# Kernel tuning notes

Measured on AMD Instinct MI355X. Metric: run time of the kernel, lower is better.

## Reference

```python
import jax, jax.numpy as jnp
import numpy as np

SEQ = 4096
EMB = 2048
DQ = 2048
DV = 2048

def setup_inputs() -> dict:
    key = jax.random.key(0)
    k1, k2, k3, k4 = jax.random.split(key, 4)
    scale = 1.0 / np.sqrt(EMB)
    return {
        "embedding_word": jax.random.normal(k1, (SEQ, EMB), dtype=jnp.float32),
        "w_q": jax.random.normal(k2, (DQ, EMB), dtype=jnp.float32) * scale,
        "w_k": jax.random.normal(k3, (DQ, EMB), dtype=jnp.float32) * scale,
        "w_v": jax.random.normal(k4, (DV, EMB), dtype=jnp.float32) * scale,
    }

def reference(embedding_word, w_q, w_k, w_v):
    # nn.Linear: y = x @ W.T (bias=False)
    q = embedding_word @ w_q.T            # [S, d_q]
    k = embedding_word @ w_k.T            # [S, d_q]
    v = embedding_word @ w_v.T            # [S, d_v]
    scores = q @ k.T                      # [S, S]
    S = scores.shape[0]
    causal = jnp.tril(jnp.ones((S, S), dtype=bool))  # True = keep
    masked = jnp.where(causal, scores, -jnp.inf)
    weights = jax.nn.softmax(masked / jnp.sqrt(jnp.float32(DQ)), axis=-1)
    return weights @ v                    # [S, d_v]
```

## Files before the change

kernel.cpp:

```cpp
#include <hip/hip_runtime.h>


using u16 = unsigned short;
typedef __bf16 bf16x8 __attribute__((ext_vector_type(8)));
typedef float  f32x4  __attribute__((ext_vector_type(4)));
typedef u16    u16x8  __attribute__((ext_vector_type(8)));

__device__ __forceinline__ u16 f2b(float f) {
  union { float f; unsigned u; } x; x.f = f;
  unsigned r = x.u + 0x7fffu + ((x.u >> 16) & 1u);
  return (u16)(r >> 16);
}
__device__ __forceinline__ float b2f(u16 h) {
  union { unsigned u; float f; } x; x.u = ((unsigned)h) << 16;
  return x.f;
}

#define GLL16(src, dst)                                                        \
  __builtin_amdgcn_global_load_lds(                                            \
      (const __attribute__((address_space(1))) void*)(src),                    \
      (__attribute__((address_space(3))) void*)(dst), 16, 0, 0)

#define MFMA_BF16(a, b, c) __builtin_amdgcn_mfma_f32_16x16x32_bf16(a, b, c, 0, 0, 0)

__global__ __launch_bounds__(256)
void cast_all(const float* __restrict__ x, const float* __restrict__ wq,
              const float* __restrict__ wk, const float* __restrict__ wv,
              u16* __restrict__ dst) {
  const int b = blockIdx.x;
  const float* src;
  size_t off;
  if (b < 4096)      { src = x;  off = (size_t)b * 2048; }
  else if (b < 6144) { src = wq; off = (size_t)(b - 4096) * 2048; }
  else if (b < 8192) { src = wk; off = (size_t)(b - 6144) * 2048; }
  else               { src = wv; off = (size_t)(b - 8192) * 2048; }
  const size_t e = off + (size_t)threadIdx.x * 8;
  float4 a = *(const float4*)(src + e);
  float4 c = *(const float4*)(src + e + 4);
  u16x8 o;
  o[0] = f2b(a.x); o[1] = f2b(a.y); o[2] = f2b(a.z); o[3] = f2b(a.w);
  o[4] = f2b(c.x); o[5] = f2b(c.y); o[6] = f2b(c.z); o[7] = f2b(c.w);
  *(u16x8*)(dst + (size_t)b * 2048 + (size_t)threadIdx.x * 8) = o;
}

__global__ __launch_bounds__(512)
void gemm_qk256(const u16* __restrict__ A, const u16* __restrict__ W,
                u16* __restrict__ Qo, u16* __restrict__ Ko) {
  extern __shared__ char lds[];
  constexpr int NT = 32;
  const int bn = blockIdx.x, bm = blockIdx.y;
  const int tid = threadIdx.x;
  const int w = tid >> 6, lane = tid & 63;
  const int wr = w >> 2, wc = w & 3;
  const int l15 = lane & 15, l4 = lane >> 4;
  const int rs = lane >> 3;
  const int csw = ((lane & 7) ^ rs) << 3;
  const int m0 = bm * 256, n0 = bn * 256;

  const u16* gA = A + (size_t)(m0 + w * 8 + rs) * 2048 + csw;
  const u16* gB = W + (size_t)(n0 + w * 8 + rs) * 2048 + csw;
  char* lw = lds + w * 1024;
  const u16* sm = (const u16*)lds;

  auto stA = [&](int p, int u, int tt) {
    GLL16(gA + (size_t)(u * 64) * 2048 + tt * 64, lw + p * 65536 + u * 8192);
  };
  auto stB = [&](int p, int u, int tt) {
    GLL16(gB + (size_t)(u * 64) * 2048 + tt * 64,
          lw + p * 65536 + 32768 + u * 8192);
  };
  const int swz = (l15 & 7) << 3;
  auto rdA = [&](int p, int m, int kk) -> bf16x8 {
    int u = wr * 2 + (m >> 2);
    int r64 = (m & 3) * 16 + l15;
    int e = p * 32768 + u * 4096 + ((r64 * 64 + kk * 32 + l4 * 8) ^ swz);
    return *(const bf16x8*)&sm[e];
  };
  auto rdB = [&](int p, int n, int kk) -> bf16x8 {
    int e = p * 32768 + 16384 + wc * 4096 +
            (((n * 16 + l15) * 64 + kk * 32 + l4 * 8) ^ swz);
    return *(const bf16x8*)&sm[e];
  };

  f32x4 acc[8][4] = {};
  bf16x8 a0[4][2], a1[4][2], b0[2][2], b1[2][2];

  stA(0,0,0); stA(0,1,0); stA(0,2,0); stA(0,3,0);
  stB(0,0,0); stB(0,1,0); stB(0,2,0); stB(0,3,0);
  stA(1,0,1); stA(1,1,1); stA(1,2,1); stA(1,3,1);
  stB(1,0,1); stB(1,1,1); stB(1,2,1); stB(1,3,1);
  asm volatile("s_waitcnt vmcnt(8)" ::: "memory");
  __builtin_amdgcn_sched_barrier(0);
  __builtin_amdgcn_s_barrier();

  for (int t = 0; t < NT; ++t) {
    const int p = t & 1;
    const bool pre = (t + 2 < NT);
#pragma unroll
    for (int m = 0; m < 4; ++m) { a0[m][0] = rdA(p, m, 0); a0[m][1] = rdA(p, m, 1); }
#pragma unroll
    for (int n = 0; n < 2; ++n) { b0[n][0] = rdB(p, n, 0); b0[n][1] = rdB(p, n, 1); }
    __builtin_amdgcn_s_barrier();
    asm volatile("s_waitcnt lgkmcnt(0)" ::: "memory");
    __builtin_amdgcn_sched_barrier(0);
    __builtin_amdgcn_s_setprio(1);
#pragma unroll
    for (int m = 0; m < 4; ++m)
#pragma unroll
      for (int n = 0; n < 2; ++n)
#pragma unroll
        for (int kk = 0; kk < 2; ++kk)
          acc[m][n] = MFMA_BF16(a0[m][kk], b0[n][kk], acc[m][n]);
    __builtin_amdgcn_s_setprio(0);
    __builtin_amdgcn_s_barrier();
    if (pre) { stA(p, 0, t + 2); stA(p, 2, t + 2); }
#pragma unroll
    for (int n = 0; n < 2; ++n) { b1[n][0] = rdB(p, n + 2, 0); b1[n][1] = rdB(p, n + 2, 1); }
    __builtin_amdgcn_s_barrier();
    asm volatile("s_waitcnt lgkmcnt(0)" ::: "memory");
    __builtin_amdgcn_sched_barrier(0);
    __builtin_amdgcn_s_setprio(1);
#pragma unroll
    for (int m = 0; m < 4; ++m)
#pragma unroll
      for (int n = 0; n < 2; ++n)
#pragma unroll
        for (int kk = 0; kk < 2; ++kk)
          acc[m][n + 2] = MFMA_BF16(a0[m][kk], b1[n][kk], acc[m][n + 2]);
    __builtin_amdgcn_s_setprio(0);
    __builtin_amdgcn_s_barrier();
    if (pre) { stB(p, 0, t + 2); stB(p, 1, t + 2); }
#pragma unroll
    for (int m = 0; m < 4; ++m) { a1[m][0] = rdA(p, m + 4, 0); a1[m][1] = rdA(p, m + 4, 1); }
    __builtin_amdgcn_s_barrier();
    asm volatile("s_waitcnt lgkmcnt(0)" ::: "memory");
    __builtin_amdgcn_sched_barrier(0);
    __builtin_amdgcn_s_setprio(1);
#pragma unroll
    for (int m = 0; m < 4; ++m)
#pragma unroll
      for (int n = 0; n < 2; ++n)
#pragma unroll
        for (int kk = 0; kk < 2; ++kk)
          acc[m + 4][n] = MFMA_BF16(a1[m][kk], b0[n][kk], acc[m + 4][n]);
    __builtin_amdgcn_s_setprio(0);
    __builtin_amdgcn_s_barrier();
    if (pre) { stA(p, 1, t + 2); stA(p, 3, t + 2); stB(p, 2, t + 2); stB(p, 3, t + 2); }
    __builtin_amdgcn_s_setprio(1);
#pragma unroll
    for (int m = 0; m < 4; ++m)
#pragma unroll
      for (int n = 0; n < 2; ++n)
#pragma unroll
        for (int kk = 0; kk < 2; ++kk)
          acc[m + 4][n + 2] = MFMA_BF16(a1[m][kk], b1[n][kk], acc[m + 4][n + 2]);
    __builtin_amdgcn_s_setprio(0);
    if (pre)                { asm volatile("s_waitcnt vmcnt(8)" ::: "memory"); }
    else if (t + 1 < NT)    { asm volatile("s_waitcnt vmcnt(0)" ::: "memory"); }
    __builtin_amdgcn_sched_barrier(0);
    __builtin_amdgcn_s_barrier();
  }

  const int row0 = m0 + wr * 128 + l4 * 4;
  if (bn < 8) {
    const int cg0 = bn * 256 + wc * 64 + l15;
#pragma unroll
    for (int m = 0; m < 8; ++m)
#pragma unroll
      for (int n = 0; n < 4; ++n)
#pragma unroll
        for (int j = 0; j < 4; ++j)
          Qo[(size_t)(row0 + m * 16 + j) * 2048 + cg0 + n * 16] = f2b(acc[m][n][j]);
  } else {
    const int cg0 = bn * 256 - 2048 + wc * 64 + l15;
#pragma unroll
    for (int m = 0; m < 8; ++m)
#pragma unroll
      for (int n = 0; n < 4; ++n)
#pragma unroll
        for (int j = 0; j < 4; ++j)
          Ko[(size_t)(row0 + m * 16 + j) * 2048 + cg0 + n * 16] = f2b(acc[m][n][j]);
  }
}

__global__ __launch_bounds__(512)
void gemm_qkv(const u16* __restrict__ A, const u16* __restrict__ W,
              u16* __restrict__ Qo, u16* __restrict__ Ko,
              u16* __restrict__ VTo, int bn_base) {
  extern __shared__ char lds[];
  constexpr int NT = 32;
  const int bn = blockIdx.x + bn_base, bm = blockIdx.y;
  const int tid = threadIdx.x;
  const int w = tid >> 6, lane = tid & 63;
  const int wr = w >> 1, wc = w & 1;
  const int l15 = lane & 15, l4 = lane >> 4;
  const int rs = lane >> 3;
  const int csw = ((lane & 7) ^ rs) << 3;
  const int m0 = bm * 256, n0 = bn * 128;

  const u16* gA = A + (size_t)(m0 + w * 8 + rs) * 2048 + csw;
  const u16* gB = W + (size_t)(n0 + w * 8 + rs) * 2048 + csw;
  char* lw = lds + w * 1024;
  const u16* sm = (const u16*)lds;

  auto stA = [&](int p, int u, int tt) {
    GLL16(gA + (size_t)u * 64 * 2048 + tt * 64, lw + p * 49152 + u * 8192);
  };
  auto stB = [&](int p, int u, int tt) {
    GLL16(gB + (size_t)u * 64 * 2048 + tt * 64, lw + p * 49152 + 32768 + u * 8192);
  };
  const int swz = (l15 & 7) << 3;
  auto rdA = [&](int p, int m, int kk) -> bf16x8 {
    int e = p * 24576 + wr * 4096 + (((m * 16 + l15) * 64 + kk * 32 + l4 * 8) ^ swz);
    return *(const bf16x8*)&sm[e];
  };
  auto rdB = [&](int p, int n, int kk) -> bf16x8 {
    int e = p * 24576 + 16384 + wc * 4096 +
            (((n * 16 + l15) * 64 + kk * 32 + l4 * 8) ^ swz);
    return *(const bf16x8*)&sm[e];
  };

  f32x4 acc[4][4] = {};
  bf16x8 aE[4][2], aO[4][2], b01E[2][2], b01O[2][2], b23E[2][2], b23O[2][2];

  stA(0,0,0); stA(0,1,0); stA(0,2,0); stA(0,3,0); stB(0,0,0); stB(0,1,0);
  stA(1,0,1); stA(1,1,1); stA(1,2,1); stA(1,3,1); stB(1,0,1); stB(1,1,1);
  asm volatile("s_waitcnt vmcnt(6)" ::: "memory");
  __builtin_amdgcn_sched_barrier(0);
  __builtin_amdgcn_s_barrier();
#pragma unroll
  for (int m = 0; m < 4; ++m) { aE[m][0] = rdA(0,m,0); aE[m][1] = rdA(0,m,1); }
#pragma unroll
  for (int n = 0; n < 2; ++n) { b01E[n][0] = rdB(0,n,0); b01E[n][1] = rdB(0,n,1); }
  asm volatile("s_waitcnt lgkmcnt(0)" ::: "memory");
  __builtin_amdgcn_sched_barrier(0);
  __builtin_amdgcn_s_barrier();

  for (int i = 0; i < NT / 2; ++i) {
    const int te = 2 * i, to = 2 * i + 1;
    if (te + 2 < NT) { stA(0,0,te+2); stA(0,1,te+2); stA(0,2,te+2); }
#pragma unroll
    for (int n = 0; n < 2; ++n) { b23E[n][0] = rdB(0,n+2,0); b23E[n][1] = rdB(0,n+2,1); }
    __builtin_amdgcn_s_barrier();
    __builtin_amdgcn_s_setprio(1);
#pragma unroll
    for (int m = 0; m < 4; ++m)
#pragma unroll
      for (int n = 0; n < 2; ++n)
#pragma unroll
        for (int kk = 0; kk < 2; ++kk)
          acc[m][n] = MFMA_BF16(aE[m][kk], b01E[n][kk], acc[m][n]);
    __builtin_amdgcn_s_setprio(0);
    asm volatile("s_waitcnt lgkmcnt(0)" ::: "memory");
    __builtin_amdgcn_sched_barrier(0);
    __builtin_amdgcn_s_barrier();
    if (te + 2 < NT) {
      stA(0,3,te+2); stB(0,0,te+2); stB(0,1,te+2);
      asm volatile("s_waitcnt vmcnt(6)" ::: "memory");
    } else {
      asm volatile("s_waitcnt vmcnt(0)" ::: "memory");
    }
    __builtin_amdgcn_sched_barrier(0);
    __builtin_amdgcn_s_barrier();
#pragma unroll
    for (int m = 0; m < 4; ++m) { aO[m][0] = rdA(1,m,0); aO[m][1] = rdA(1,m,1); }
#pragma unroll
    for (int n = 0; n < 2; ++n) { b01O[n][0] = rdB(1,n,0); b01O[n][1] = rdB(1,n,1); }
    __builtin_amdgcn_s_setprio(1);
#pragma unroll
    for (int m = 0; m < 4; ++m)
#pragma unroll
      for (int n = 0; n < 2; ++n)
#pragma unroll
        for (int kk = 0; kk < 2; ++kk)
          acc[m][n+2] = MFMA_BF16(aE[m][kk], b23E[n][kk], acc[m][n+2]);
    __builtin_amdgcn_s_setprio(0);
    asm volatile("s_waitcnt lgkmcnt(0)" ::: "memory");
    __builtin_amdgcn_sched_barrier(0);
    __builtin_amdgcn_s_barrier();
    if (to + 2 < NT) { stA(1,0,to+2); stA(1,1,to+2); stA(1,2,to+2); }
#pragma unroll
    for (int n = 0; n < 2; ++n) { b23O[n][0] = rdB(1,n+2,0); b23O[n][1] = rdB(1,n+2,1); }
    __builtin_amdgcn_s_barrier();
    __builtin_amdgcn_s_setprio(1);
#pragma unroll
    for (int m = 0; m < 4; ++m)
#pragma unroll
      for (int n = 0; n < 2; ++n)
#pragma unroll
        for (int kk = 0; kk < 2; ++kk)
          acc[m][n] = MFMA_BF16(aO[m][kk], b01O[n][kk], acc[m][n]);
    __builtin_amdgcn_s_setprio(0);
    asm volatile("s_waitcnt lgkmcnt(0)" ::: "memory");
    __builtin_amdgcn_sched_barrier(0);
    __builtin_amdgcn_s_barrier();
    if (to + 2 < NT) {
      stA(1,3,to+2); stB(1,0,to+2); stB(1,1,to+2);
      asm volatile("s_waitcnt vmcnt(6)" ::: "memory");
    } else if (to + 1 < NT) {
      asm volatile("s_waitcnt vmcnt(0)" ::: "memory");
    }
    __builtin_amdgcn_sched_barrier(0);
    __builtin_amdgcn_s_barrier();
    if (to + 1 < NT) {
#pragma unroll
      for (int m = 0; m < 4; ++m) { aE[m][0] = rdA(0,m,0); aE[m][1] = rdA(0,m,1); }
#pragma unroll
      for (int n = 0; n < 2; ++n) { b01E[n][0] = rdB(0,n,0); b01E[n][1] = rdB(0,n,1); }
    }
    __builtin_amdgcn_s_setprio(1);
#pragma unroll
    for (int m = 0; m < 4; ++m)
#pragma unroll
      for (int n = 0; n < 2; ++n)
#pragma unroll
        for (int kk = 0; kk < 2; ++kk)
          acc[m][n+2] = MFMA_BF16(aO[m][kk], b23O[n][kk], acc[m][n+2]);
    __builtin_amdgcn_s_setprio(0);
    asm volatile("s_waitcnt lgkmcnt(0)" ::: "memory");
    __builtin_amdgcn_sched_barrier(0);
    __builtin_amdgcn_s_barrier();
  }

  const int row0 = m0 + wr * 64 + l4 * 4;
  const int cg0 = n0 + wc * 64 + l15;
  if (bn < 16) {
#pragma unroll
    for (int m = 0; m < 4; ++m)
#pragma unroll
      for (int n = 0; n < 4; ++n)
#pragma unroll
        for (int j = 0; j < 4; ++j)
          Qo[(size_t)(row0 + m * 16 + j) * 2048 + cg0 + n * 16] = f2b(acc[m][n][j]);
  } else if (bn < 32) {
#pragma unroll
    for (int m = 0; m < 4; ++m)
#pragma unroll
      for (int n = 0; n < 4; ++n)
#pragma unroll
        for (int j = 0; j < 4; ++j)
          Ko[(size_t)(row0 + m * 16 + j) * 2048 + (cg0 + n * 16 - 2048)] = f2b(acc[m][n][j]);
  } else {
#pragma unroll
    for (int m = 0; m < 4; ++m)
#pragma unroll
      for (int n = 0; n < 4; ++n)
#pragma unroll
        for (int j = 0; j < 4; ++j)
          VTo[(size_t)(cg0 + n * 16 - 4096) * 4096 + row0 + m * 16 + j] = f2b(acc[m][n][j]);
  }
}

template<int MODE>
__global__ __launch_bounds__(256)
void pipe128(const u16* __restrict__ A, const u16* __restrict__ B,
             void* __restrict__ C, float alpha) {
  extern __shared__ char lds[];
  constexpr int LDA = (MODE == 0) ? 2048 : 4096;
  constexpr int LDB = (MODE == 0) ? 2048 : 4096;

  int bm, bn;
  if (MODE == 0) {
    const int b = blockIdx.x;
    int r = (int)((sqrtf(8.f * (float)b + 1.f) - 1.f) * 0.5f);
    while ((r + 1) * (r + 2) / 2 <= b) ++r;
    while (r * (r + 1) / 2 > b) --r;
    bm = r; bn = b - r * (r + 1) / 2;
  } else {
    const int b = blockIdx.x;
    const int i = b >> 1;
    bm = (b & 1) ? (31 - (i >> 4)) : (i >> 4);
    bn = i & 15;
  }
  const int NT = (MODE == 0) ? 32 : 2 * (bm + 1);

  const int tid = threadIdx.x;
  const int w = tid >> 6, lane = tid & 63;
  const int wr = w >> 1, wc = w & 1;
  const int l15 = lane & 15, l4 = lane >> 4;
  const int rs = lane >> 3;
  const int csw = ((lane & 7) ^ rs) << 3;
  const int m0 = bm * 128, n0 = bn * 128;

  const u16* gA = A + (size_t)(m0 + w * 8 + rs) * LDA + csw;
  const u16* gB = B + (size_t)(n0 + w * 8 + rs) * LDB + csw;
  char* lw = lds + w * 1024;
  const u16* sm = (const u16*)lds;

  auto stA = [&](int p, int u, int tt) {
    GLL16(gA + (size_t)(u * 32) * LDA + tt * 64, lw + p * 32768 + u * 4096);
  };
  auto stB = [&](int p, int u, int tt) {
    GLL16(gB + (size_t)(u * 32) * LDB + tt * 64, lw + p * 32768 + 16384 + u * 4096);
  };
  const int swz = (l15 & 7) << 3;
  auto rdA = [&](int p, int m, int kk) -> bf16x8 {
    int e = p * 16384 + wr * 4096 + (((m * 16 + l15) * 64 + kk * 32 + l4 * 8) ^ swz);
    return *(const bf16x8*)&sm[e];
  };
  auto rdB = [&](int p, int n, int kk) -> bf16x8 {
    int e = p * 16384 + 8192 + wc * 4096 +
            (((n * 16 + l15) * 64 + kk * 32 + l4 * 8) ^ swz);
    return *(const bf16x8*)&sm[e];
  };

  f32x4 acc[4][4] = {};
  bf16x8 aE[4][2], aO[4][2], b01E[2][2], b01O[2][2], b23E[2][2], b23O[2][2];

  stA(0,0,0); stA(0,1,0); stA(0,2,0); stA(0,3,0);
  stB(0,0,0); stB(0,1,0); stB(0,2,0); stB(0,3,0);
  stA(1,0,1); stA(1,1,1); stA(1,2,1); stA(1,3,1);
  stB(1,0,1); stB(1,1,1); stB(1,2,1); stB(1,3,1);
  asm volatile("s_waitcnt vmcnt(8)" ::: "memory");
  __builtin_amdgcn_sched_barrier(0);
  __builtin_amdgcn_s_barrier();
#pragma unroll
  for (int m = 0; m < 4; ++m) { aE[m][0] = rdA(0,m,0); aE[m][1] = rdA(0,m,1); }
#pragma unroll
  for (int n = 0; n < 2; ++n) { b01E[n][0] = rdB(0,n,0); b01E[n][1] = rdB(0,n,1); }
  asm volatile("s_waitcnt lgkmcnt(0)" ::: "memory");
  __builtin_amdgcn_sched_barrier(0);
  __builtin_amdgcn_s_barrier();

  for (int i = 0; i < (NT >> 1); ++i) {
    const int te = 2 * i, to = 2 * i + 1;
    if (te + 2 < NT) { stA(0,0,te+2); stA(0,1,te+2); stA(0,2,te+2); stA(0,3,te+2); }
#pragma unroll
    for (int n = 0; n < 2; ++n) { b23E[n][0] = rdB(0,n+2,0); b23E[n][1] = rdB(0,n+2,1); }
    __builtin_amdgcn_s_barrier();
    __builtin_amdgcn_s_setprio(1);
#pragma unroll
    for (int m = 0; m < 4; ++m)
#pragma unroll
      for (int n = 0; n < 2; ++n)
#pragma unroll
        for (int kk = 0; kk < 2; ++kk)
          acc[m][n] = MFMA_BF16(aE[m][kk], b01E[n][kk], acc[m][n]);
    __builtin_amdgcn_s_setprio(0);
    asm volatile("s_waitcnt lgkmcnt(0)" ::: "memory");
    __builtin_amdgcn_sched_barrier(0);
    __builtin_amdgcn_s_barrier();
    if (te + 2 < NT) {
      stB(0,0,te+2); stB(0,1,te+2); stB(0,2,te+2); stB(0,3,te+2);
      asm volatile("s_waitcnt vmcnt(8)" ::: "memory");
    } else {
      asm volatile("s_waitcnt vmcnt(0)" ::: "memory");
    }
    __builtin_amdgcn_sched_barrier(0);
    __builtin_amdgcn_s_barrier();
#pragma unroll
    for (int m = 0; m < 4; ++m) { aO[m][0] = rdA(1,m,0); aO[m][1] = rdA(1,m,1); }
#pragma unroll
    for (int n = 0; n < 2; ++n) { b01O[n][0] = rdB(1,n,0); b01O[n][1] = rdB(1,n,1); }
    __builtin_amdgcn_s_setprio(1);
#pragma unroll
    for (int m = 0; m < 4; ++m)
#pragma unroll
      for (int n = 0; n < 2; ++n)
#pragma unroll
        for (int kk = 0; kk < 2; ++kk)
          acc[m][n+2] = MFMA_BF16(aE[m][kk], b23E[n][kk], acc[m][n+2]);
    __builtin_amdgcn_s_setprio(0);
    asm volatile("s_waitcnt lgkmcnt(0)" ::: "memory");
    __builtin_amdgcn_sched_barrier(0);
    __builtin_amdgcn_s_barrier();
    if (to + 2 < NT) { stA(1,0,to+2); stA(1,1,to+2); stA(1,2,to+2); stA(1,3,to+2); }
#pragma unroll
    for (int n = 0; n < 2; ++n) { b23O[n][0] = rdB(1,n+2,0); b23O[n][1] = rdB(1,n+2,1); }
    __builtin_amdgcn_s_barrier();
    __builtin_amdgcn_s_setprio(1);
#pragma unroll
    for (int m = 0; m < 4; ++m)
#pragma unroll
      for (int n = 0; n < 2; ++n)
#pragma unroll
        for (int kk = 0; kk < 2; ++kk)
          acc[m][n] = MFMA_BF16(aO[m][kk], b01O[n][kk], acc[m][n]);
    __builtin_amdgcn_s_setprio(0);
    asm volatile("s_waitcnt lgkmcnt(0)" ::: "memory");
    __builtin_amdgcn_sched_barrier(0);
    __builtin_amdgcn_s_barrier();
    if (to + 2 < NT) {
      stB(1,0,to+2); stB(1,1,to+2); stB(1,2,to+2); stB(1,3,to+2);
      asm volatile("s_waitcnt vmcnt(8)" ::: "memory");
    } else if (to + 1 < NT) {
      asm volatile("s_waitcnt vmcnt(0)" ::: "memory");
    }
    __builtin_amdgcn_sched_barrier(0);
    __builtin_amdgcn_s_barrier();
    if (to + 1 < NT) {
#pragma unroll
      for (int m = 0; m < 4; ++m) { aE[m][0] = rdA(0,m,0); aE[m][1] = rdA(0,m,1); }
#pragma unroll
      for (int n = 0; n < 2; ++n) { b01E[n][0] = rdB(0,n,0); b01E[n][1] = rdB(0,n,1); }
    }
    __builtin_amdgcn_s_setprio(1);
#pragma unroll
    for (int m = 0; m < 4; ++m)
#pragma unroll
      for (int n = 0; n < 2; ++n)
#pragma unroll
        for (int kk = 0; kk < 2; ++kk)
          acc[m][n+2] = MFMA_BF16(aO[m][kk], b23O[n][kk], acc[m][n+2]);
    __builtin_amdgcn_s_setprio(0);
    asm volatile("s_waitcnt lgkmcnt(0)" ::: "memory");
    __builtin_amdgcn_sched_barrier(0);
    __builtin_amdgcn_s_barrier();
  }

  const int row0 = m0 + wr * 64 + l4 * 4;
  const int col0 = n0 + wc * 64 + l15;
  if (MODE == 0) {
    u16* Co = (u16*)C;
#pragma unroll
    for (int m = 0; m < 4; ++m)
#pragma unroll
      for (int n = 0; n < 4; ++n)
#pragma unroll
        for (int j = 0; j < 4; ++j)
          Co[(size_t)(row0 + m * 16 + j) * 4096 + col0 + n * 16] =
              f2b(acc[m][n][j] * alpha);
  } else {
    float* Co = (float*)C;
#pragma unroll
    for (int m = 0; m < 4; ++m)
#pragma unroll
      for (int n = 0; n < 4; ++n)
#pragma unroll
        for (int j = 0; j < 4; ++j)
          Co[(size_t)(row0 + m * 16 + j) * 2048 + col0 + n * 16] = acc[m][n][j];
  }
}

__global__ __launch_bounds__(256)
void softmax_causal(u16* __restrict__ S) {
  const int i = blockIdx.x;
  const int t = threadIdx.x;
  u16* row = S + (size_t)i * 4096;

  u16x8 r0 = *(const u16x8*)(row + t * 16);
  u16x8 r1 = *(const u16x8*)(row + t * 16 + 8);

  float v[16];
  float mx = -__builtin_inff();
#pragma unroll
  for (int c = 0; c < 16; ++c) {
    int j = t * 16 + c;
    float x = b2f(c < 8 ? r0[c] : r1[c - 8]);
    v[c] = (j <= i) ? x : -__builtin_inff();
    mx = fmaxf(mx, v[c]);
  }
#pragma unroll
  for (int off = 32; off >= 1; off >>= 1) mx = fmaxf(mx, __shfl_xor(mx, off));
  __shared__ float red[8];
  if ((t & 63) == 0) red[t >> 6] = mx;
  __syncthreads();
  mx = fmaxf(fmaxf(red[0], red[1]), fmaxf(red[2], red[3]));

  float s = 0.f;
#pragma unroll
  for (int c = 0; c < 16; ++c) {
    float e = exp2f((v[c] - mx) * 1.4426950408889634f);
    v[c] = e;
    s += e;
  }
#pragma unroll
  for (int off = 32; off >= 1; off >>= 1) s += __shfl_xor(s, off);
  if ((t & 63) == 0) red[4 + (t >> 6)] = s;
  __syncthreads();
  s = red[4] + red[5] + red[6] + red[7];
  float inv = 1.0f / s;

  u16x8 o0, o1;
#pragma unroll
  for (int c = 0; c < 8; ++c) {
    o0[c] = f2b(v[c] * inv);
    o1[c] = f2b(v[c + 8] * inv);
  }
  *(u16x8*)(row + t * 16) = o0;
  *(u16x8*)(row + t * 16 + 8) = o1;
}

extern "C" void kernel_launch(void* const* d_in, const int* in_sizes, int n_in,
                              void* d_out, int out_size, void* d_ws, size_t ws_size,
                              hipStream_t stream) {
  const float* x  = (const float*)d_in[0];
  const float* wq = (const float*)d_in[1];
  const float* wk = (const float*)d_in[2];
  const float* wv = (const float*)d_in[3];

  u16* x_bf  = (u16*)d_ws;
  u16* wq_bf = x_bf  + (size_t)4096 * 2048;
  u16* K_bf  = wq_bf + (size_t)3 * 2048 * 2048;
  u16* VT_bf = K_bf  + (size_t)4096 * 2048;
  u16* S_bf  = VT_bf + (size_t)2048 * 4096;
  u16* Q_bf  = (u16*)d_out;

  const float alpha = 0.022097086912079612f;

  cast_all<<<dim3(10240), 256, 0, stream>>>(x, wq, wk, wv, x_bf);

  gemm_qk256<<<dim3(16, 16), 512, 131072, stream>>>(x_bf, wq_bf, Q_bf, K_bf);
  pipe128<0><<<dim3(528), 256, 65536, stream>>>(Q_bf, K_bf, S_bf, alpha);
  gemm_qkv<<<dim3(16, 16), 512, 98304, stream>>>(x_bf, wq_bf, Q_bf, K_bf, VT_bf, 32);
  softmax_causal<<<dim3(4096), 256, 0, stream>>>(S_bf);
  pipe128<1><<<dim3(512), 256, 65536, stream>>>(S_bf, VT_bf, d_out, 1.0f);
}
```

Measured before the change: 260.2 us.

## Split causal PV GEMM into two launches to balance lower-triangle work

The final weights@V GEMM now runs as two launches. The first covers the lower row blocks (16-31) over the first half of K (32 tiles). The second covers the remaining causal K range for those rows and accumulates into the output with +=, while also handling the upper row blocks (0-15) in full. Work per block is then capped at 32 K-tiles instead of up to 64, which shortens the tail of the imbalanced triangular schedule. The cost is an extra launch plus a read-modify-write of half the fp32 output.

```diff
diff --git a/kernel.cpp b/kernel.cpp
--- a/kernel.cpp
+++ b/kernel.cpp
@@ -359,20 +359,23 @@
   constexpr int LDA = (MODE == 0) ? 2048 : 4096;
   constexpr int LDB = (MODE == 0) ? 2048 : 4096;
 
-  int bm, bn;
+  int bm, bn, kt0 = 0;
+  bool accum = false;
   if (MODE == 0) {
     const int b = blockIdx.x;
     int r = (int)((sqrtf(8.f * (float)b + 1.f) - 1.f) * 0.5f);
     while ((r + 1) * (r + 2) / 2 <= b) ++r;
     while (r * (r + 1) / 2 > b) --r;
     bm = r; bn = b - r * (r + 1) / 2;
+  } else if (MODE == 1) {
+    bm = 16 + (blockIdx.x >> 4); bn = blockIdx.x & 15;
   } else {
-    const int b = blockIdx.x;
-    const int i = b >> 1;
-    bm = (b & 1) ? (31 - (i >> 4)) : (i >> 4);
-    bn = i & 15;
-  }
-  const int NT = (MODE == 0) ? 32 : 2 * (bm + 1);
+    const int g = blockIdx.x >> 4;
+    bn = blockIdx.x & 15;
+    if ((g & 1) == 0) { bm = 31 - (g >> 1); kt0 = 32; accum = true; }
+    else              { bm = 15 - (g >> 1); }
+  }
+  const int NT = (MODE == 0 || MODE == 1) ? 32 : (2 * (bm + 1) - kt0);
 
   const int tid = threadIdx.x;
   const int w = tid >> 6, lane = tid & 63;
@@ -382,8 +385,8 @@
   const int csw = ((lane & 7) ^ rs) << 3;
   const int m0 = bm * 128, n0 = bn * 128;
 
-  const u16* gA = A + (size_t)(m0 + w * 8 + rs) * LDA + csw;
-  const u16* gB = B + (size_t)(n0 + w * 8 + rs) * LDB + csw;
+  const u16* gA = A + (size_t)(m0 + w * 8 + rs) * LDA + csw + (size_t)kt0 * 64;
+  const u16* gB = B + (size_t)(n0 + w * 8 + rs) * LDB + csw + (size_t)kt0 * 64;
   char* lw = lds + w * 1024;
   const u16* sm = (const u16*)lds;
 
@@ -522,13 +525,23 @@
               f2b(acc[m][n][j] * alpha);
   } else {
     float* Co = (float*)C;
-#pragma unroll
-    for (int m = 0; m < 4; ++m)
-#pragma unroll
-      for (int n = 0; n < 4; ++n)
-#pragma unroll
-        for (int j = 0; j < 4; ++j)
-          Co[(size_t)(row0 + m * 16 + j) * 2048 + col0 + n * 16] = acc[m][n][j];
+    if (MODE == 2 && accum) {
+#pragma unroll
+      for (int m = 0; m < 4; ++m)
+#pragma unroll
+        for (int n = 0; n < 4; ++n)
+#pragma unroll
+          for (int j = 0; j < 4; ++j)
+            Co[(size_t)(row0 + m * 16 + j) * 2048 + col0 + n * 16] += acc[m][n][j];
+    } else {
+#pragma unroll
+      for (int m = 0; m < 4; ++m)
+#pragma unroll
+        for (int n = 0; n < 4; ++n)
+#pragma unroll
+          for (int j = 0; j < 4; ++j)
+            Co[(size_t)(row0 + m * 16 + j) * 2048 + col0 + n * 16] = acc[m][n][j];
+    }
   }
 }
 
@@ -604,5 +617,6 @@
   pipe128<0><<<dim3(528), 256, 65536, stream>>>(Q_bf, K_bf, S_bf, alpha);
   gemm_qkv<<<dim3(16, 16), 512, 98304, stream>>>(x_bf, wq_bf, Q_bf, K_bf, VT_bf, 32);
   softmax_causal<<<dim3(4096), 256, 0, stream>>>(S_bf);
-  pipe128<1><<<dim3(512), 256, 65536, stream>>>(S_bf, VT_bf, d_out, 1.0f);
-}
+  pipe128<1><<<dim3(256), 256, 65536, stream>>>(S_bf, VT_bf, d_out, 1.0f);
+  pipe128<2><<<dim3(512), 256, 65536, stream>>>(S_bf, VT_bf, d_out, 1.0f);
+}
```

After: 244.3 us. 6.1% less time.
